# Performance work log

Hardware: AMD Instinct MI355X
Metric: run time of the kernel (lower is better)

The kernel has to match this reference:

```python
import jax, jax.numpy as jnp
import numpy as np
from jax import lax

HID = 256
CB_N = 512   # codebook_size
CB_D = 64    # codebook_dim
FC = 6       # force_channels
COMMIT_W = 0.25


def _conv(x, w, b, stride):
    # x: [B,C,H,W], w: [O,I,3,3], 'same'-style padding=1
    y = lax.conv_general_dilated(x, w, (stride, stride), ((1, 1), (1, 1)),
                                 dimension_numbers=('NCHW', 'OIHW', 'NCHW'))
    return y + b[None, :, None, None]


def _silu(x):
    return x * jax.nn.sigmoid(x)


def setup_inputs() -> dict:
    key = jax.random.key(0)
    ks = jax.random.split(key, 8)
    s = 0.05
    force_field = jax.random.normal(ks[0], (8, FC, 256, 256), dtype=jnp.float32)
    w1 = jax.random.normal(ks[1], (HID, FC, 3, 3), dtype=jnp.float32) * s
    b1 = jnp.zeros((HID,), dtype=jnp.float32)
    w2 = jax.random.normal(ks[2], (HID, HID, 3, 3), dtype=jnp.float32) * s
    b2 = jnp.zeros((HID,), dtype=jnp.float32)
    w3 = jax.random.normal(ks[3], (CB_D, HID, 3, 3), dtype=jnp.float32) * s
    b3 = jnp.zeros((CB_D,), dtype=jnp.float32)
    codebook = jax.random.uniform(ks[4], (CB_N, CB_D), dtype=jnp.float32,
                                  minval=-1.0 / CB_N, maxval=1.0 / CB_N)
    return {"force_field": force_field, "w1": w1, "b1": b1, "w2": w2,
            "b2": b2, "w3": w3, "b3": b3, "codebook": codebook}


def reference(force_field, w1, b1, w2, b2, w3, b3, codebook):
    # Encoder: conv(pad1) -> SiLU -> conv(stride2) -> SiLU -> conv(stride2)
    h = _silu(_conv(force_field, w1, b1, 1))
    h = _silu(_conv(h, w2, b2, 2))
    z = _conv(h, w3, b3, 2)                      # [B, CB_D, h, w]
    B, C, hh, ww = z.shape
    z_flat = jnp.transpose(z, (0, 2, 3, 1)).reshape(-1, C)  # [N, CB_D]
    # pairwise squared distances: ||z||^2 + ||c||^2 - 2 z.c
    dists = (jnp.sum(z_flat * z_flat, axis=1, keepdims=True)
             + jnp.sum(codebook * codebook, axis=1)
             - 2.0 * (z_flat @ codebook.T))      # [N, CB_N]
    indices = jnp.argmin(dists, axis=1)          # [N] int
    z_q = codebook[indices].reshape(B, hh, ww, C).transpose(0, 3, 1, 2)
    commitment_loss = (jnp.mean((lax.stop_gradient(z_q) - z) ** 2)
                       + COMMIT_W * jnp.mean((z_q - lax.stop_gradient(z)) ** 2))
    tokens = indices.reshape(B, hh, ww)
    return tokens, commitment_loss
```

## Files before the change

kernel.cpp:

```cpp
#include <hip/hip_runtime.h>
#include <math.h>


#define FC    6
#define HID   256
#define CB_N  512
#define CB_D  64

typedef _Float16 f16x8 __attribute__((ext_vector_type(8)));
typedef _Float16 f16x4 __attribute__((ext_vector_type(4)));
typedef float f32x16 __attribute__((ext_vector_type(16)));

#define H1N_IMG    17105920
#define H2N_IMG    4359168

#define FFP_ROW    260
#define FFP_CI     (258 * FFP_ROW)
#define FFP_IMG    (6 * FFP_CI)

__global__ void fill_sentinel_kernel(float* out, int n) {
    int i = blockIdx.x * 256 + threadIdx.x;
    if (i < n) out[i] = -12345.0f;
}

__global__ void guards_kernel(unsigned int* h1n, unsigned int* h2n, int nslots) {
    int i = blockIdx.x * 256 + threadIdx.x;
    const int n1 = nslots * 132096;
    if (i < n1) {
        int slot = i / 132096;
        int r    = i - slot * 132096;
        unsigned int* base = h1n + (size_t)slot * H1N_IMG;
        if (r < 66560) base[r] = 0u;
        else {
            int r2  = r - 66560;
            int j   = r2 & 3;
            int hl  = (r2 >> 2) & 1;
            int cg  = (r2 >> 3) & 31;
            int row = (r2 >> 8) + 1;
            base[(size_t)row * 66560 + 33280 + cg * 1040 + hl * 520 + j] = 0u;
        }
        return;
    }
    i -= n1;
    if (i >= nslots * 66560) return;
    int slot = i / 66560;
    int r    = i - slot * 66560;
    unsigned int* base = h2n + (size_t)slot * H2N_IMG;
    if (r < 33792) base[r] = 0u;
    else {
        int r2  = r - 33792;
        int j   = r2 & 3;
        int hl  = (r2 >> 2) & 1;
        int cg  = (r2 >> 3) & 31;
        int row = (r2 >> 8) + 1;
        base[(size_t)row * 33792 + 16896 + cg * 528 + hl * 264 + j] = 0u;
    }
}

__global__ void wswz1_kernel(const float* __restrict__ w1, _Float16* __restrict__ wsz) {
    int i = blockIdx.x * 256 + threadIdx.x;
    if (i >= 2 * 4 * 4096) return;
    int j   = i & 7;
    int co_ = (i >> 3) & 127;
    int kc  = (i >> 10) & 1;
    int hf  = (i >> 11) & 1;
    int st  = (i >> 12) & 3;
    int ct  = i >> 14;
    int k   = st * 16 + kc * 8 + j;
    int co  = ct * 128 + co_;
    float v = (k < 54) ? w1[(size_t)co * 54 + k] : 0.f;
    _Float16 h = (_Float16)v;
    _Float16 l = (_Float16)(v - (float)h);
    wsz[i] = hf ? l : h;
}

__global__ void wswz2_kernel(const float* __restrict__ w2, _Float16* __restrict__ wsz) {
    int i = blockIdx.x * 256 + threadIdx.x;
    if (i >= 2 * 144 * 4096) return;
    int j   = i & 7;
    int co_ = (i >> 3) & 127;
    int kc  = (i >> 10) & 1;
    int hf  = (i >> 11) & 1;
    int st  = (i >> 12) % 144;
    int ct  = (i >> 12) / 144;
    int ci  = (st & 15) * 16 + kc * 8 + j;
    int rs  = st >> 4;
    float v = w2[(size_t)(ct * 128 + co_) * 2304 + ci * 9 + rs];
    _Float16 h = (_Float16)v;
    _Float16 l = (_Float16)(v - (float)h);
    wsz[i] = hf ? l : h;
}

__global__ void wswz3_kernel(const float* __restrict__ w3, _Float16* __restrict__ wsz) {
    int i = blockIdx.x * 256 + threadIdx.x;
    if (i >= 144 * 2048) return;
    int j  = i & 7;
    int co = (i >> 3) & 63;
    int kc = (i >> 9) & 1;
    int hf = (i >> 10) & 1;
    int st = i >> 11;
    int ci = (st & 15) * 16 + kc * 8 + j;
    int rs = st >> 4;
    float v = w3[(size_t)co * 2304 + ci * 9 + rs];
    _Float16 h = (_Float16)v;
    _Float16 l = (_Float16)(v - (float)h);
    wsz[i] = hf ? l : h;
}

__global__ void cnorm_kernel(const float* __restrict__ cb, float* __restrict__ cn) {
    int j = blockIdx.x * 256 + threadIdx.x;
    if (j < CB_N) {
        const float* p = cb + j * CB_D;
        float s0 = 0.f, s1 = 0.f, s2 = 0.f, s3 = 0.f;
        for (int i = 0; i < CB_D; i += 4) {
            s0 = fmaf(p[i],   p[i],   s0);
            s1 = fmaf(p[i+1], p[i+1], s1);
            s2 = fmaf(p[i+2], p[i+2], s2);
            s3 = fmaf(p[i+3], p[i+3], s3);
        }
        cn[j] = (s0 + s1) + (s2 + s3);
    }
}

__device__ __forceinline__ float silu_f(float v) {
    return v / (1.f + expf(-v));
}

__device__ __forceinline__ unsigned int pack_hl(float v) {
    _Float16 h = (_Float16)v;
    _Float16 l = (_Float16)(v - (float)h);
    unsigned short hb = __builtin_bit_cast(unsigned short, h);
    unsigned short lb = __builtin_bit_cast(unsigned short, l);
    return (unsigned int)hb | ((unsigned int)lb << 16);
}

__device__ __forceinline__ f16x8 as_f16x8(uint4 v) {
    return __builtin_bit_cast(f16x8, v);
}

__device__ __forceinline__ unsigned int ldu32_sb(const char* base, unsigned off, int px) {
    return *(const unsigned int*)(base + (unsigned)__builtin_amdgcn_readfirstlane((int)off) + px * 4);
}

__device__ __forceinline__ void sync_lds() {
    asm volatile("s_waitcnt lgkmcnt(0)\n\ts_barrier" ::: "memory");
}

__global__ __launch_bounds__(256) void ffpack_kernel(const float* __restrict__ ff,
                                                     unsigned int* __restrict__ ffp) {
    const int gw   = (blockIdx.x * 256 + threadIdx.x) >> 6;
    const int lane = threadIdx.x & 63;
    const int y  = gw & 255;
    const int ic = gw >> 8;
    const float* rowp = ff + ((size_t)ic * 256 + y) * 256;
    float4 v = *(const float4*)(rowp + 4 * lane);
    unsigned p0 = pack_hl(v.x), p1 = pack_hl(v.y), p2 = pack_hl(v.z), p3 = pack_hl(v.w);
    unsigned p3p = __shfl_up(p3, 1);
    if (lane == 0) p3p = 0u;
    unsigned int* orow = ffp + ((size_t)ic * 258 + y + 1) * FFP_ROW;
    uint4 o; o.x = p3p; o.y = p0; o.z = p1; o.w = p2;
    *(uint4*)(orow + 4 * lane) = o;
    if (lane == 63) { orow[256] = p3; orow[257] = 0u; }
}

__global__ __launch_bounds__(256) void conv1_mfma_kernel(
        const unsigned int* __restrict__ ffp,
        const _Float16* __restrict__ wsz1,
        const float* __restrict__ bias,
        unsigned int* __restrict__ h1n,
        int b0) {
    __shared__ __align__(16) _Float16 ldsA[2][2][128][8];
    __shared__ __align__(16) _Float16 ldsB[2][128][24];
    __shared__ __align__(16) unsigned int T[64];
    __shared__ float biasl[128];

    const int tid = threadIdx.x;
    const int py  = blockIdx.x >> 1;
    const int xt  = blockIdx.x & 1;
    const int ct  = blockIdx.y;
    const int img = blockIdx.z;

    const unsigned int* ffpi = ffp + (size_t)(b0 + img) * FFP_IMG;
    _Float16* h1f = (_Float16*)(h1n + (size_t)img * H1N_IMG);

    if (tid < 64) {
        int k = tid;
        unsigned off;
        if (k < 54) {
            int ci  = k / 9;
            int tap = k - ci * 9;
            int r   = tap / 3;
            int s   = tap - r * 3;
            off = (unsigned)((((size_t)ci * 258 + py + r) * FFP_ROW + xt * 128 + s) * 4);
        } else {
            off = (unsigned)((xt * 128) * 4);
        }
        T[k] = off;
    }
    if (tid < 128) biasl[tid] = bias[ct * 128 + tid];
    __syncthreads();

    const int lane = tid & 63;
    const int w    = tid >> 6;
    const int cow  = (w >> 1) * 64;
    const int pxw  = (w & 1) * 64;
    const int m_   = lane & 31;
    const int kc   = lane >> 5;
    const int px   = tid & 127;
    const int kh   = tid >> 7;

    f32x16 acc[2][2];
    #pragma unroll
    for (int a = 0; a < 2; a++)
        #pragma unroll
        for (int b = 0; b < 2; b++)
            #pragma unroll
            for (int r = 0; r < 16; r++) acc[a][b][r] = 0.f;

    uint4* aldsf = (uint4*)&ldsA[0][0][0][0];
    const char* gbase = (const char*)ffpi;

    uint4 a0, a1;
    unsigned v0, v1, v2, v3, v4, v5, v6, v7;
    {
        const uint4* ag = (const uint4*)(wsz1 + ((size_t)(ct * 4)) * 4096);
        a0 = ag[tid];
        a1 = ag[tid + 256];
        const int k0 = kh * 8;
        uint4 rb0 = *(const uint4*)&T[k0];
        uint4 rb1 = *(const uint4*)&T[k0 + 4];
        v0 = ldu32_sb(gbase, rb0.x, px); v1 = ldu32_sb(gbase, rb0.y, px);
        v2 = ldu32_sb(gbase, rb0.z, px); v3 = ldu32_sb(gbase, rb0.w, px);
        v4 = ldu32_sb(gbase, rb1.x, px); v5 = ldu32_sb(gbase, rb1.y, px);
        v6 = ldu32_sb(gbase, rb1.z, px); v7 = ldu32_sb(gbase, rb1.w, px);
    }

    for (int t = 0; t < 4; t++) {
        sync_lds();

        aldsf[tid]       = a0;
        aldsf[tid + 256] = a1;
        uint4 bh, bl;
        bh.x = (v0 & 0xffffu) | (v1 << 16);
        bh.y = (v2 & 0xffffu) | (v3 << 16);
        bh.z = (v4 & 0xffffu) | (v5 << 16);
        bh.w = (v6 & 0xffffu) | (v7 << 16);
        bl.x = (v0 >> 16) | (v1 & 0xffff0000u);
        bl.y = (v2 >> 16) | (v3 & 0xffff0000u);
        bl.z = (v4 >> 16) | (v5 & 0xffff0000u);
        bl.w = (v6 >> 16) | (v7 & 0xffff0000u);
        *(uint4*)&ldsB[0][px][kh * 8] = bh;
        *(uint4*)&ldsB[1][px][kh * 8] = bl;

        sync_lds();

        if (t < 3) {
            const uint4* ag = (const uint4*)(wsz1 + ((size_t)(ct * 4 + t + 1)) * 4096);
            a0 = ag[tid];
            a1 = ag[tid + 256];
            const int k0 = (t + 1) * 16 + kh * 8;
            uint4 rb0 = *(const uint4*)&T[k0 & 63];
            uint4 rb1 = *(const uint4*)&T[(k0 + 4) & 63];
            v0 = ldu32_sb(gbase, rb0.x, px); v1 = ldu32_sb(gbase, rb0.y, px);
            v2 = ldu32_sb(gbase, rb0.z, px); v3 = ldu32_sb(gbase, rb0.w, px);
            v4 = ldu32_sb(gbase, rb1.x, px); v5 = ldu32_sb(gbase, rb1.y, px);
            v6 = ldu32_sb(gbase, rb1.z, px); v7 = ldu32_sb(gbase, rb1.w, px);
        }

        f16x8 ah0 = *(const f16x8*)&ldsA[0][kc][cow + m_][0];
        f16x8 ah1 = *(const f16x8*)&ldsA[0][kc][cow + 32 + m_][0];
        f16x8 al0 = *(const f16x8*)&ldsA[1][kc][cow + m_][0];
        f16x8 al1 = *(const f16x8*)&ldsA[1][kc][cow + 32 + m_][0];
        f16x8 xh0 = *(const f16x8*)&ldsB[0][pxw + m_][kc * 8];
        f16x8 xh1 = *(const f16x8*)&ldsB[0][pxw + 32 + m_][kc * 8];
        f16x8 xl0 = *(const f16x8*)&ldsB[1][pxw + m_][kc * 8];
        f16x8 xl1 = *(const f16x8*)&ldsB[1][pxw + 32 + m_][kc * 8];

        acc[0][0] = __builtin_amdgcn_mfma_f32_32x32x16_f16(ah0, xh0, acc[0][0], 0, 0, 0);
        acc[0][1] = __builtin_amdgcn_mfma_f32_32x32x16_f16(ah0, xh1, acc[0][1], 0, 0, 0);
        acc[1][0] = __builtin_amdgcn_mfma_f32_32x32x16_f16(ah1, xh0, acc[1][0], 0, 0, 0);
        acc[1][1] = __builtin_amdgcn_mfma_f32_32x32x16_f16(ah1, xh1, acc[1][1], 0, 0, 0);
        acc[0][0] = __builtin_amdgcn_mfma_f32_32x32x16_f16(ah0, xl0, acc[0][0], 0, 0, 0);
        acc[0][1] = __builtin_amdgcn_mfma_f32_32x32x16_f16(ah0, xl1, acc[0][1], 0, 0, 0);
        acc[1][0] = __builtin_amdgcn_mfma_f32_32x32x16_f16(ah1, xl0, acc[1][0], 0, 0, 0);
        acc[1][1] = __builtin_amdgcn_mfma_f32_32x32x16_f16(ah1, xl1, acc[1][1], 0, 0, 0);
        acc[0][0] = __builtin_amdgcn_mfma_f32_32x32x16_f16(al0, xh0, acc[0][0], 0, 0, 0);
        acc[0][1] = __builtin_amdgcn_mfma_f32_32x32x16_f16(al0, xh1, acc[0][1], 0, 0, 0);
        acc[1][0] = __builtin_amdgcn_mfma_f32_32x32x16_f16(al1, xh0, acc[1][0], 0, 0, 0);
        acc[1][1] = __builtin_amdgcn_mfma_f32_32x32x16_f16(al1, xh1, acc[1][1], 0, 0, 0);
    }

    #pragma unroll
    for (int mt = 0; mt < 2; mt++) {
        #pragma unroll
        for (int nt = 0; nt < 2; nt++) {
            const int pxo = xt * 128 + pxw + nt * 32 + m_;
            const int par = pxo & 1;
            const int xs  = par ? ((pxo + 1) >> 1) : (pxo >> 1);
            _Float16* dst = h1f + (size_t)(py + 1) * 133120 + par * 66560 + xs * 8 + kc * 4;
            #pragma unroll
            for (int q = 0; q < 4; q++) {
                const int cb_ = cow + mt * 32 + 8 * q + 4 * kc;
                const int cg  = (ct * 128 + cow + mt * 32 + 8 * q) >> 3;
                f16x4 oh, ol;
                #pragma unroll
                for (int j = 0; j < 4; j++) {
                    float v = silu_f(acc[mt][nt][4*q+j] + biasl[cb_ + j]);
                    _Float16 h = (_Float16)v;
                    oh[j] = h;
                    ol[j] = (_Float16)(v - (float)h);
                }
                *(f16x4*)(dst + (size_t)cg * 2080)        = oh;
                *(f16x4*)(dst + (size_t)cg * 2080 + 1040) = ol;
            }
        }
    }
}

__global__ __launch_bounds__(256) void conv2_mfma_kernel(
        const unsigned int* __restrict__ h1n,
        const _Float16* __restrict__ wsz2,
        const float* __restrict__ bias,
        unsigned int* __restrict__ h2n) {
    __shared__ __align__(16) char ldsB[2 * 16384];
    __shared__ float biasl[128];

    const int tid = threadIdx.x;
    const int py  = blockIdx.x;
    const int ct  = blockIdx.y;
    const int img = blockIdx.z;

    if (tid < 128) biasl[tid] = bias[ct * 128 + tid];

    const int lane = tid & 63;
    const int w    = tid >> 6;
    const int cow  = (w >> 1) * 64;
    const int pxw  = (w & 1) * 64;
    const int m_   = lane & 31;
    const int kc   = lane >> 5;

    const char* bbase = (const char*)(h1n + (size_t)img * H1N_IMG);
    const char* abase = (const char*)wsz2 + (size_t)ct * 144 * 8192
                        + (size_t)kc * 2048 + (size_t)(cow + m_) * 16;

    const int spx = tid & 127;
    const int skc = tid >> 7;
    const unsigned sgfix = (unsigned)(skc * 4160 + spx * 16);
    const unsigned swfix = (unsigned)(skc * 2048 + spx * 16);
    const unsigned rfix0 = (unsigned)(kc * 2048 + (pxw + m_) * 16);
    const unsigned rfix1 = (unsigned)(kc * 2048 + (pxw + 32 + m_) * 16);

    auto offu = [&](int t) -> unsigned {
        int rs = t >> 4;
        int r  = (rs * 11) >> 5;
        int s  = rs - 3 * r;
        return (unsigned)((2 * py + r) * 266240 + (s != 1 ? 133120 : 0)
                          + (s == 2 ? 16 : 0) + (t & 15) * 8320);
    };

    f32x16 acc[2][2];
    #pragma unroll
    for (int a = 0; a < 2; a++)
        #pragma unroll
        for (int b = 0; b < 2; b++)
            #pragma unroll
            for (int r = 0; r < 16; r++) acc[a][b][r] = 0.f;

    uint4 pa0, pa1, pa2, pa3;
    uint4 wa0, wa1, wa2, wa3;
    uint4 wb0, wb1, wb2, wb3;
    {
        pa0 = *(const uint4*)(abase);
        pa1 = *(const uint4*)(abase + 512);
        pa2 = *(const uint4*)(abase + 4096);
        pa3 = *(const uint4*)(abase + 4096 + 512);
        unsigned o0 = offu(0);
        uint4 th = *(const uint4*)(bbase + o0 + sgfix);
        uint4 tl = *(const uint4*)(bbase + o0 + sgfix + 2080);
        *(uint4*)(ldsB + swfix)        = th;
        *(uint4*)(ldsB + 4096 + swfix) = tl;
        unsigned o1 = offu(1);
        th = *(const uint4*)(bbase + o1 + sgfix);
        tl = *(const uint4*)(bbase + o1 + sgfix + 2080);
        *(uint4*)(ldsB + 8192 + swfix)  = th;
        *(uint4*)(ldsB + 12288 + swfix) = tl;
        unsigned o2 = offu(2);
        wa0 = *(const uint4*)(bbase + o2 + sgfix);
        wa1 = *(const uint4*)(bbase + o2 + sgfix + 2080);
        unsigned o3 = offu(3);
        wa2 = *(const uint4*)(bbase + o3 + sgfix);
        wa3 = *(const uint4*)(bbase + o3 + sgfix + 2080);
        unsigned o4 = offu(4);
        wb0 = *(const uint4*)(bbase + o4 + sgfix);
        wb1 = *(const uint4*)(bbase + o4 + sgfix + 2080);
        unsigned o5 = offu(5);
        wb2 = *(const uint4*)(bbase + o5 + sgfix);
        wb3 = *(const uint4*)(bbase + o5 + sgfix + 2080);
    }
    sync_lds();

    auto superstep = [&](int s, uint4& W0, uint4& W1, uint4& W2, uint4& W3) {
        const int t0 = 2 * s;
        char* rslot = ldsB + (s & 1) * 16384;

        if (s < 71) {
            char* wslot = ldsB + ((s + 1) & 1) * 16384;
            *(uint4*)(wslot + swfix)         = W0;
            *(uint4*)(wslot + 4096 + swfix)  = W1;
            *(uint4*)(wslot + 8192 + swfix)  = W2;
            *(uint4*)(wslot + 12288 + swfix) = W3;
        }
        if (s < 69) {
            unsigned oa = offu(t0 + 6);
            unsigned ob = offu(t0 + 7);
            W0 = *(const uint4*)(bbase + oa + sgfix);
            W1 = *(const uint4*)(bbase + oa + sgfix + 2080);
            W2 = *(const uint4*)(bbase + ob + sgfix);
            W3 = *(const uint4*)(bbase + ob + sgfix + 2080);
        }

        f16x8 xh0 = *(const f16x8*)(rslot + rfix0);
        f16x8 xl0 = *(const f16x8*)(rslot + 4096 + rfix0);
        f16x8 xh1 = *(const f16x8*)(rslot + rfix1);
        f16x8 xl1 = *(const f16x8*)(rslot + 4096 + rfix1);

        uint4 ca0 = pa0, ca1 = pa1, ca2 = pa2, ca3 = pa3;
        {
            const char* ap = abase + (size_t)(t0 + 1) * 8192;
            pa0 = *(const uint4*)(ap);
            pa1 = *(const uint4*)(ap + 512);
            pa2 = *(const uint4*)(ap + 4096);
            pa3 = *(const uint4*)(ap + 4096 + 512);
        }

        f16x8 ah0 = as_f16x8(ca0);
        f16x8 ah1 = as_f16x8(ca1);
        f16x8 al0 = as_f16x8(ca2);
        f16x8 al1 = as_f16x8(ca3);

        acc[0][0] = __builtin_amdgcn_mfma_f32_32x32x16_f16(ah0, xh0, acc[0][0], 0, 0, 0);
        acc[0][1] = __builtin_amdgcn_mfma_f32_32x32x16_f16(ah0, xh1, acc[0][1], 0, 0, 0);
        acc[1][0] = __builtin_amdgcn_mfma_f32_32x32x16_f16(ah1, xh0, acc[1][0], 0, 0, 0);
        acc[1][1] = __builtin_amdgcn_mfma_f32_32x32x16_f16(ah1, xh1, acc[1][1], 0, 0, 0);
        acc[0][0] = __builtin_amdgcn_mfma_f32_32x32x16_f16(ah0, xl0, acc[0][0], 0, 0, 0);
        acc[0][1] = __builtin_amdgcn_mfma_f32_32x32x16_f16(ah0, xl1, acc[0][1], 0, 0, 0);
        acc[1][0] = __builtin_amdgcn_mfma_f32_32x32x16_f16(ah1, xl0, acc[1][0], 0, 0, 0);
        acc[1][1] = __builtin_amdgcn_mfma_f32_32x32x16_f16(ah1, xl1, acc[1][1], 0, 0, 0);
        acc[0][0] = __builtin_amdgcn_mfma_f32_32x32x16_f16(al0, xh0, acc[0][0], 0, 0, 0);
        acc[0][1] = __builtin_amdgcn_mfma_f32_32x32x16_f16(al0, xh1, acc[0][1], 0, 0, 0);
        acc[1][0] = __builtin_amdgcn_mfma_f32_32x32x16_f16(al1, xh0, acc[1][0], 0, 0, 0);
        acc[1][1] = __builtin_amdgcn_mfma_f32_32x32x16_f16(al1, xh1, acc[1][1], 0, 0, 0);

        f16x8 yh0 = *(const f16x8*)(rslot + 8192 + rfix0);
        f16x8 yl0 = *(const f16x8*)(rslot + 12288 + rfix0);
        f16x8 yh1 = *(const f16x8*)(rslot + 8192 + rfix1);
        f16x8 yl1 = *(const f16x8*)(rslot + 12288 + rfix1);

        ca0 = pa0; ca1 = pa1; ca2 = pa2; ca3 = pa3;
        if (s < 71) {
            const char* ap = abase + (size_t)(t0 + 2) * 8192;
            pa0 = *(const uint4*)(ap);
            pa1 = *(const uint4*)(ap + 512);
            pa2 = *(const uint4*)(ap + 4096);
            pa3 = *(const uint4*)(ap + 4096 + 512);
        }

        ah0 = as_f16x8(ca0);
        ah1 = as_f16x8(ca1);
        al0 = as_f16x8(ca2);
        al1 = as_f16x8(ca3);

        acc[0][0] = __builtin_amdgcn_mfma_f32_32x32x16_f16(ah0, yh0, acc[0][0], 0, 0, 0);
        acc[0][1] = __builtin_amdgcn_mfma_f32_32x32x16_f16(ah0, yh1, acc[0][1], 0, 0, 0);
        acc[1][0] = __builtin_amdgcn_mfma_f32_32x32x16_f16(ah1, yh0, acc[1][0], 0, 0, 0);
        acc[1][1] = __builtin_amdgcn_mfma_f32_32x32x16_f16(ah1, yh1, acc[1][1], 0, 0, 0);
        acc[0][0] = __builtin_amdgcn_mfma_f32_32x32x16_f16(ah0, yl0, acc[0][0], 0, 0, 0);
        acc[0][1] = __builtin_amdgcn_mfma_f32_32x32x16_f16(ah0, yl1, acc[0][1], 0, 0, 0);
        acc[1][0] = __builtin_amdgcn_mfma_f32_32x32x16_f16(ah1, yl0, acc[1][0], 0, 0, 0);
        acc[1][1] = __builtin_amdgcn_mfma_f32_32x32x16_f16(ah1, yl1, acc[1][1], 0, 0, 0);
        acc[0][0] = __builtin_amdgcn_mfma_f32_32x32x16_f16(al0, yh0, acc[0][0], 0, 0, 0);
        acc[0][1] = __builtin_amdgcn_mfma_f32_32x32x16_f16(al0, yh1, acc[0][1], 0, 0, 0);
        acc[1][0] = __builtin_amdgcn_mfma_f32_32x32x16_f16(al1, yh0, acc[1][0], 0, 0, 0);
        acc[1][1] = __builtin_amdgcn_mfma_f32_32x32x16_f16(al1, yh1, acc[1][1], 0, 0, 0);

        sync_lds();
    };

    for (int ss = 0; ss < 36; ss++) {
        superstep(2 * ss,     wa0, wa1, wa2, wa3);
        superstep(2 * ss + 1, wb0, wb1, wb2, wb3);
    }

    _Float16* h2f = (_Float16*)(h2n + (size_t)img * H2N_IMG);
    #pragma unroll
    for (int mt = 0; mt < 2; mt++) {
        #pragma unroll
        for (int nt = 0; nt < 2; nt++) {
            const int pxo = pxw + nt * 32 + m_;
            const int par = pxo & 1;
            const int xs  = par ? ((pxo + 1) >> 1) : (pxo >> 1);
            _Float16* dst = h2f + (size_t)(py + 1) * 67584 + par * 33792 + xs * 8 + kc * 4;
            #pragma unroll
            for (int q = 0; q < 4; q++) {
                const int cb_ = cow + mt * 32 + 8 * q + 4 * kc;
                const int cg  = (ct * 128 + cow + mt * 32 + 8 * q) >> 3;
                f16x4 oh, ol;
                #pragma unroll
                for (int j = 0; j < 4; j++) {
                    float v = silu_f(acc[mt][nt][4*q+j] + biasl[cb_ + j]);
                    _Float16 h = (_Float16)v;
                    oh[j] = h;
                    ol[j] = (_Float16)(v - (float)h);
                }
                *(f16x4*)(dst + (size_t)cg * 1056)       = oh;
                *(f16x4*)(dst + (size_t)cg * 1056 + 528) = ol;
            }
        }
    }
}

__global__ __launch_bounds__(64) void conv3_mfma_kernel(
        const unsigned int* __restrict__ h2n,
        const _Float16* __restrict__ wsz3,
        const float* __restrict__ bias,
        float* __restrict__ z) {
    const int bi  = blockIdx.x;
    const int img = blockIdx.y;
    const int py  = bi >> 2;
    const int ct3 = (bi >> 1) & 1;
    const int pxt = bi & 1;

    const int lane = threadIdx.x;
    const int m_   = lane & 31;
    const int kc   = lane >> 5;

    const char* bbase = (const char*)(h2n + (size_t)img * H2N_IMG);
    const char* abase = (const char*)wsz3 + (size_t)kc * 1024 + (size_t)(ct3 * 32 + m_) * 16;
    const unsigned bfix = (unsigned)(kc * 2112 + (pxt * 32 + m_) * 16);

    auto offu = [&](int t) -> unsigned {
        int rs = t >> 4;
        int r  = (rs * 11) >> 5;
        int s  = rs - 3 * r;
        return (unsigned)((2 * py + r) * 135168 + (s != 1 ? 67584 : 0)
                          + (s == 2 ? 16 : 0) + (t & 15) * 4224);
    };

    f32x16 acc;
    #pragma unroll
    for (int r = 0; r < 16; r++) acc[r] = 0.f;

    uint4 rh[8], rl[8];
    #pragma unroll
    for (int i = 0; i < 8; i++) {
        unsigned o = offu(i);
        rh[i] = *(const uint4*)(bbase + o + bfix);
        rl[i] = *(const uint4*)(bbase + o + bfix + 1056);
    }
    uint4 pa0 = *(const uint4*)(abase);
    uint4 pa1 = *(const uint4*)(abase + 2048);

    for (int tb = 0; tb < 144; tb += 8) {
        #pragma unroll
        for (int i = 0; i < 8; i++) {
            const int t = tb + i;
            uint4 cbh = rh[i], cbl = rl[i];
            if (t + 8 < 144) {
                unsigned o = offu(t + 8);
                rh[i] = *(const uint4*)(bbase + o + bfix);
                rl[i] = *(const uint4*)(bbase + o + bfix + 1056);
            }
            uint4 ca0 = pa0, ca1 = pa1;
            if (t < 143) {
                const char* ap = abase + (size_t)(t + 1) * 4096;
                pa0 = *(const uint4*)(ap);
                pa1 = *(const uint4*)(ap + 2048);
            }
            f16x8 ah = as_f16x8(ca0);
            f16x8 al = as_f16x8(ca1);
            f16x8 xh = as_f16x8(cbh);
            f16x8 xl = as_f16x8(cbl);
            acc = __builtin_amdgcn_mfma_f32_32x32x16_f16(ah, xh, acc, 0, 0, 0);
            acc = __builtin_amdgcn_mfma_f32_32x32x16_f16(ah, xl, acc, 0, 0, 0);
            acc = __builtin_amdgcn_mfma_f32_32x32x16_f16(al, xh, acc, 0, 0, 0);
        }
    }

    const int x = pxt * 32 + m_;
    float* zp = z + (((size_t)img * 64 + py) * 64 + x) * 64;
    #pragma unroll
    for (int q = 0; q < 4; q++) {
        const int co = ct3 * 32 + 8 * q + 4 * kc;
        float4 o;
        o.x = acc[4*q+0] + bias[co + 0];
        o.y = acc[4*q+1] + bias[co + 1];
        o.z = acc[4*q+2] + bias[co + 2];
        o.w = acc[4*q+3] + bias[co + 3];
        *(float4*)(zp + co) = o;
    }
}

__global__ __launch_bounds__(128) void vqfused_kernel(const float* __restrict__ z,
                                                      const float* __restrict__ cb,
                                                      const float* __restrict__ cn,
                                                      float* __restrict__ tokens_out,
                                                      float* __restrict__ loss_accum) {
    __shared__ __align__(16) float lds_cb[128 * 64];
    __shared__ float lds_cn[128];
    __shared__ float red[2];

    const int tid = threadIdx.x;
    const int n   = blockIdx.x * 128 + tid;

    float zr[64];
    const float* zp = z + (size_t)n * 64;
    #pragma unroll
    for (int i = 0; i < 16; i++)
        *(float4*)&zr[i * 4] = *(const float4*)(zp + i * 4);

    float zn0 = 0.f, zn1 = 0.f, zn2 = 0.f, zn3 = 0.f;
    #pragma unroll
    for (int i = 0; i < 64; i += 4) {
        zn0 = fmaf(zr[i],   zr[i],   zn0);
        zn1 = fmaf(zr[i+1], zr[i+1], zn1);
        zn2 = fmaf(zr[i+2], zr[i+2], zn2);
        zn3 = fmaf(zr[i+3], zr[i+3], zn3);
    }
    const float znorm = (zn0 + zn1) + (zn2 + zn3);

    float dmin = 1e30f;
    int best = 0;

    for (int q = 0; q < 4; q++) {
        if (q) __syncthreads();
        #pragma unroll
        for (int i = 0; i < 16; i++) {
            const int f4 = tid + 128 * i;
            *(float4*)&lds_cb[f4 * 4] = *(const float4*)(cb + q * 8192 + f4 * 4);
        }
        lds_cn[tid] = cn[q * 128 + tid];
        __syncthreads();

        for (int j = 0; j < 128; j++) {
            const float* cp = &lds_cb[j * 64];
            float d0 = 0.f, d1 = 0.f, d2 = 0.f, d3 = 0.f;
            #pragma unroll
            for (int i = 0; i < 16; i++) {
                const float4 c4 = *(const float4*)&cp[i * 4];
                d0 = fmaf(zr[i*4],   c4.x, d0);
                d1 = fmaf(zr[i*4+1], c4.y, d1);
                d2 = fmaf(zr[i*4+2], c4.z, d2);
                d3 = fmaf(zr[i*4+3], c4.w, d3);
            }
            const float dot = (d0 + d1) + (d2 + d3);
            const float d = (znorm + lds_cn[j]) - 2.f * dot;
            if (d < dmin) { dmin = d; best = q * 128 + j; }
        }
    }

    tokens_out[n] = (float)best;

    const float* cbest = cb + (size_t)best * 64;
    float l0 = 0.f, l1 = 0.f, l2 = 0.f, l3 = 0.f;
    #pragma unroll
    for (int i = 0; i < 64; i += 4) {
        float t0 = cbest[i]     - zr[i];
        float t1 = cbest[i + 1] - zr[i + 1];
        float t2 = cbest[i + 2] - zr[i + 2];
        float t3 = cbest[i + 3] - zr[i + 3];
        l0 = fmaf(t0, t0, l0);
        l1 = fmaf(t1, t1, l1);
        l2 = fmaf(t2, t2, l2);
        l3 = fmaf(t3, t3, l3);
    }
    float l = (l0 + l1) + (l2 + l3);
    #pragma unroll
    for (int off = 32; off > 0; off >>= 1)
        l += __shfl_down(l, off);
    if ((tid & 63) == 0) red[tid >> 6] = l;
    __syncthreads();
    if (tid == 0)
        atomicAdd(loss_accum, red[0] + red[1]);
}

__global__ void finalize_kernel(const float* __restrict__ loss_accum,
                                float* __restrict__ out_loss) {
    const float m = loss_accum[0] / 2097152.f;
    out_loss[0] = m + 0.25f * m;
}

extern "C" void kernel_launch(void* const* d_in, const int* in_sizes, int n_in,
                              void* d_out, int out_size, void* d_ws, size_t ws_size,
                              hipStream_t stream) {
    const float* ff = (const float*)d_in[0];
    const float* w1 = (const float*)d_in[1];
    const float* b1 = (const float*)d_in[2];
    const float* w2 = (const float*)d_in[3];
    const float* b2 = (const float*)d_in[4];
    const float* w3 = (const float*)d_in[5];
    const float* b3 = (const float*)d_in[6];
    const float* cb = (const float*)d_in[7];
    float* out = (float*)d_out;
    float* ws  = (float*)d_ws;

    const size_t TAIL = 2097152 + 8 * (size_t)FFP_IMG + 589824 + 147456 + 16384
                      + 512 + 131072 + 131072 + 1;
    auto need_u32 = [&](int nimg) -> size_t {
        return (size_t)nimg * (H1N_IMG + H2N_IMG) + TAIL;
    };

    int nimg;
    if      (ws_size >= need_u32(8) * 4) nimg = 8;
    else if (ws_size >= need_u32(4) * 4) nimg = 4;
    else if (ws_size >= need_u32(2) * 4) nimg = 2;
    else {
        fill_sentinel_kernel<<<(out_size + 255) / 256, 256, 0, stream>>>(out, out_size);
        return;
    }

    unsigned int* h1n  = (unsigned int*)ws;
    unsigned int* h2n  = h1n + (size_t)nimg * H1N_IMG;
    float*        zbuf = (float*)(h2n + (size_t)nimg * H2N_IMG);
    unsigned int* ffp  = (unsigned int*)(zbuf + 2097152);
    _Float16* wsz2 = (_Float16*)(ffp + 8 * (size_t)FFP_IMG);
    _Float16* wsz3 = wsz2 + 1179648;
    _Float16* wsz1 = wsz3 + 294912;
    float*    cn   = (float*)(wsz1 + 32768);
    float*    pd   = cn + 512;
    int*      pi   = (int*)(pd + 131072);
    float*    lacc = (float*)(pi + 131072);

    hipMemsetAsync(ffp, 0, 8 * (size_t)FFP_IMG * 4, stream);
    guards_kernel<<<(nimg * (132096 + 66560) + 255) / 256, 256, 0, stream>>>(h1n, h2n, nimg);
    wswz1_kernel<<<(2 * 4 * 4096 + 255) / 256, 256, 0, stream>>>(w1, wsz1);
    wswz2_kernel<<<(2 * 144 * 4096 + 255) / 256, 256, 0, stream>>>(w2, wsz2);
    wswz3_kernel<<<(144 * 2048 + 255) / 256, 256, 0, stream>>>(w3, wsz3);
    cnorm_kernel<<<2, 256, 0, stream>>>(cb, cn);
    ffpack_kernel<<<3072, 256, 0, stream>>>(ff, ffp);

    for (int b0 = 0; b0 < 8; b0 += nimg) {
        conv1_mfma_kernel<<<dim3(512, 2, nimg), 256, 0, stream>>>(ffp, wsz1, b1, h1n, b0);
        conv2_mfma_kernel<<<dim3(128, 2, nimg), 256, 0, stream>>>(h1n, wsz2, b2, h2n);
        conv3_mfma_kernel<<<dim3(256, nimg), 64, 0, stream>>>(
            h2n, wsz3, b3, zbuf + (size_t)b0 * 262144);
    }

    hipMemsetAsync(lacc, 0, sizeof(float), stream);
    vqfused_kernel<<<256, 128, 0, stream>>>(zbuf, cb, cn, out, lacc);
    finalize_kernel<<<1, 1, 0, stream>>>(lacc, out + 32768);
}
```

Baseline: 953.4 us.

## Split VQ codebook search across two half-blocks and merge prep kernels

The VQ kernel now runs 256 threads per block. Each half searches a different 256-entry half of the codebook for the same 128 vectors, then the two halves merge their minima through shared memory. This doubles the active waves in the latency-bound argmin stage, at the cost of each thread loading its z row twice and an extra sync. The four weight-swizzle and codebook-norm kernels are also fused into one launch, and the image batch size can now be any value from 2 to 8 depending on workspace.

```diff
diff --git a/kernel.cpp b/kernel.cpp
--- a/kernel.cpp
+++ b/kernel.cpp
@@ -57,68 +57,68 @@
     }
 }
 
-__global__ void wswz1_kernel(const float* __restrict__ w1, _Float16* __restrict__ wsz) {
+__global__ void prep_kernel(const float* __restrict__ w1, const float* __restrict__ w2,
+                            const float* __restrict__ w3, const float* __restrict__ cbk,
+                            _Float16* __restrict__ wsz1, _Float16* __restrict__ wsz2,
+                            _Float16* __restrict__ wsz3, float* __restrict__ cn) {
     int i = blockIdx.x * 256 + threadIdx.x;
-    if (i >= 2 * 4 * 4096) return;
-    int j   = i & 7;
-    int co_ = (i >> 3) & 127;
-    int kc  = (i >> 10) & 1;
-    int hf  = (i >> 11) & 1;
-    int st  = (i >> 12) & 3;
-    int ct  = i >> 14;
-    int k   = st * 16 + kc * 8 + j;
-    int co  = ct * 128 + co_;
-    float v = (k < 54) ? w1[(size_t)co * 54 + k] : 0.f;
-    _Float16 h = (_Float16)v;
-    _Float16 l = (_Float16)(v - (float)h);
-    wsz[i] = hf ? l : h;
-}
-
-__global__ void wswz2_kernel(const float* __restrict__ w2, _Float16* __restrict__ wsz) {
-    int i = blockIdx.x * 256 + threadIdx.x;
-    if (i >= 2 * 144 * 4096) return;
-    int j   = i & 7;
-    int co_ = (i >> 3) & 127;
-    int kc  = (i >> 10) & 1;
-    int hf  = (i >> 11) & 1;
-    int st  = (i >> 12) % 144;
-    int ct  = (i >> 12) / 144;
-    int ci  = (st & 15) * 16 + kc * 8 + j;
-    int rs  = st >> 4;
-    float v = w2[(size_t)(ct * 128 + co_) * 2304 + ci * 9 + rs];
-    _Float16 h = (_Float16)v;
-    _Float16 l = (_Float16)(v - (float)h);
-    wsz[i] = hf ? l : h;
-}
-
-__global__ void wswz3_kernel(const float* __restrict__ w3, _Float16* __restrict__ wsz) {
-    int i = blockIdx.x * 256 + threadIdx.x;
-    if (i >= 144 * 2048) return;
-    int j  = i & 7;
-    int co = (i >> 3) & 63;
-    int kc = (i >> 9) & 1;
-    int hf = (i >> 10) & 1;
-    int st = i >> 11;
-    int ci = (st & 15) * 16 + kc * 8 + j;
-    int rs = st >> 4;
-    float v = w3[(size_t)co * 2304 + ci * 9 + rs];
-    _Float16 h = (_Float16)v;
-    _Float16 l = (_Float16)(v - (float)h);
-    wsz[i] = hf ? l : h;
-}
-
-__global__ void cnorm_kernel(const float* __restrict__ cb, float* __restrict__ cn) {
-    int j = blockIdx.x * 256 + threadIdx.x;
-    if (j < CB_N) {
-        const float* p = cb + j * CB_D;
+    if (i < 32768) {
+        int j   = i & 7;
+        int co_ = (i >> 3) & 127;
+        int kc  = (i >> 10) & 1;
+        int hf  = (i >> 11) & 1;
+        int st  = (i >> 12) & 3;
+        int ct  = i >> 14;
+        int k   = st * 16 + kc * 8 + j;
+        int co  = ct * 128 + co_;
+        float v = (k < 54) ? w1[(size_t)co * 54 + k] : 0.f;
+        _Float16 h = (_Float16)v;
+        _Float16 l = (_Float16)(v - (float)h);
+        wsz1[i] = hf ? l : h;
+        return;
+    }
+    i -= 32768;
+    if (i < 2 * 144 * 4096) {
+        int j   = i & 7;
+        int co_ = (i >> 3) & 127;
+        int kc  = (i >> 10) & 1;
+        int hf  = (i >> 11) & 1;
+        int st  = (i >> 12) % 144;
+        int ct  = (i >> 12) / 144;
+        int ci  = (st & 15) * 16 + kc * 8 + j;
+        int rs  = st >> 4;
+        float v = w2[(size_t)(ct * 128 + co_) * 2304 + ci * 9 + rs];
+        _Float16 h = (_Float16)v;
+        _Float16 l = (_Float16)(v - (float)h);
+        wsz2[i] = hf ? l : h;
+        return;
+    }
+    i -= 2 * 144 * 4096;
+    if (i < 144 * 2048) {
+        int j  = i & 7;
+        int co = (i >> 3) & 63;
+        int kc = (i >> 9) & 1;
+        int hf = (i >> 10) & 1;
+        int st = i >> 11;
+        int ci = (st & 15) * 16 + kc * 8 + j;
+        int rs = st >> 4;
+        float v = w3[(size_t)co * 2304 + ci * 9 + rs];
+        _Float16 h = (_Float16)v;
+        _Float16 l = (_Float16)(v - (float)h);
+        wsz3[i] = hf ? l : h;
+        return;
+    }
+    i -= 144 * 2048;
+    if (i < CB_N) {
+        const float* p = cbk + i * CB_D;
         float s0 = 0.f, s1 = 0.f, s2 = 0.f, s3 = 0.f;
-        for (int i = 0; i < CB_D; i += 4) {
-            s0 = fmaf(p[i],   p[i],   s0);
-            s1 = fmaf(p[i+1], p[i+1], s1);
-            s2 = fmaf(p[i+2], p[i+2], s2);
-            s3 = fmaf(p[i+3], p[i+3], s3);
-        }
-        cn[j] = (s0 + s1) + (s2 + s3);
+        for (int k = 0; k < CB_D; k += 4) {
+            s0 = fmaf(p[k],   p[k],   s0);
+            s1 = fmaf(p[k+1], p[k+1], s1);
+            s2 = fmaf(p[k+2], p[k+2], s2);
+            s3 = fmaf(p[k+3], p[k+3], s3);
+        }
+        cn[i] = (s0 + s1) + (s2 + s3);
     }
 }
 
@@ -600,17 +600,21 @@
     }
 }
 
-__global__ __launch_bounds__(128) void vqfused_kernel(const float* __restrict__ z,
+__global__ __launch_bounds__(256) void vqfused_kernel(const float* __restrict__ z,
                                                       const float* __restrict__ cb,
                                                       const float* __restrict__ cn,
                                                       float* __restrict__ tokens_out,
                                                       float* __restrict__ loss_accum) {
-    __shared__ __align__(16) float lds_cb[128 * 64];
-    __shared__ float lds_cn[128];
-    __shared__ float red[2];
-
-    const int tid = threadIdx.x;
-    const int n   = blockIdx.x * 128 + tid;
+    __shared__ __align__(16) float lds_cb[2][64 * 64];
+    __shared__ float lds_cn[2][64];
+    __shared__ float lds_d[128];
+    __shared__ int   lds_i[128];
+    __shared__ float red[4];
+
+    const int tid  = threadIdx.x;
+    const int half = tid >> 7;
+    const int ltid = tid & 127;
+    const int n    = blockIdx.x * 128 + ltid;
 
     float zr[64];
     const float* zp = z + (size_t)n * 64;
@@ -631,18 +635,19 @@
     float dmin = 1e30f;
     int best = 0;
 
-    for (int q = 0; q < 4; q++) {
-        if (q) __syncthreads();
+    for (int st = 0; st < 4; st++) {
+        const int c0 = half * 256 + st * 64;
+        if (st) __syncthreads();
         #pragma unroll
-        for (int i = 0; i < 16; i++) {
-            const int f4 = tid + 128 * i;
-            *(float4*)&lds_cb[f4 * 4] = *(const float4*)(cb + q * 8192 + f4 * 4);
-        }
-        lds_cn[tid] = cn[q * 128 + tid];
+        for (int i = 0; i < 8; i++) {
+            const int f4 = ltid + 128 * i;
+            *(float4*)&lds_cb[half][f4 * 4] = *(const float4*)(cb + (size_t)c0 * 64 + f4 * 4);
+        }
+        if (ltid < 64) lds_cn[half][ltid] = cn[c0 + ltid];
         __syncthreads();
 
-        for (int j = 0; j < 128; j++) {
-            const float* cp = &lds_cb[j * 64];
+        for (int j = 0; j < 64; j++) {
+            const float* cp = &lds_cb[half][j * 64];
             float d0 = 0.f, d1 = 0.f, d2 = 0.f, d3 = 0.f;
             #pragma unroll
             for (int i = 0; i < 16; i++) {
@@ -653,34 +658,43 @@
                 d3 = fmaf(zr[i*4+3], c4.w, d3);
             }
             const float dot = (d0 + d1) + (d2 + d3);
-            const float d = (znorm + lds_cn[j]) - 2.f * dot;
-            if (d < dmin) { dmin = d; best = q * 128 + j; }
-        }
-    }
-
-    tokens_out[n] = (float)best;
-
-    const float* cbest = cb + (size_t)best * 64;
-    float l0 = 0.f, l1 = 0.f, l2 = 0.f, l3 = 0.f;
-    #pragma unroll
-    for (int i = 0; i < 64; i += 4) {
-        float t0 = cbest[i]     - zr[i];
-        float t1 = cbest[i + 1] - zr[i + 1];
-        float t2 = cbest[i + 2] - zr[i + 2];
-        float t3 = cbest[i + 3] - zr[i + 3];
-        l0 = fmaf(t0, t0, l0);
-        l1 = fmaf(t1, t1, l1);
-        l2 = fmaf(t2, t2, l2);
-        l3 = fmaf(t3, t3, l3);
-    }
-    float l = (l0 + l1) + (l2 + l3);
+            const float d = (znorm + lds_cn[half][j]) - 2.f * dot;
+            if (d < dmin) { dmin = d; best = c0 + j; }
+        }
+    }
+
+    if (half) { lds_d[ltid] = dmin; lds_i[ltid] = best; }
+    __syncthreads();
+
+    float l = 0.f;
+    if (half == 0) {
+        const float d1 = lds_d[ltid];
+        const int   i1 = lds_i[ltid];
+        if (d1 < dmin) { dmin = d1; best = i1; }
+        tokens_out[n] = (float)best;
+
+        const float* cbest = cb + (size_t)best * 64;
+        float l0 = 0.f, l1 = 0.f, l2 = 0.f, l3 = 0.f;
+        #pragma unroll
+        for (int i = 0; i < 64; i += 4) {
+            float t0 = cbest[i]     - zr[i];
+            float t1 = cbest[i + 1] - zr[i + 1];
+            float t2 = cbest[i + 2] - zr[i + 2];
+            float t3 = cbest[i + 3] - zr[i + 3];
+            l0 = fmaf(t0, t0, l0);
+            l1 = fmaf(t1, t1, l1);
+            l2 = fmaf(t2, t2, l2);
+            l3 = fmaf(t3, t3, l3);
+        }
+        l = (l0 + l1) + (l2 + l3);
+    }
     #pragma unroll
     for (int off = 32; off > 0; off >>= 1)
         l += __shfl_down(l, off);
     if ((tid & 63) == 0) red[tid >> 6] = l;
     __syncthreads();
     if (tid == 0)
-        atomicAdd(loss_accum, red[0] + red[1]);
+        atomicAdd(loss_accum, (red[0] + red[1]) + (red[2] + red[3]));
 }
 
 __global__ void finalize_kernel(const float* __restrict__ loss_accum,
@@ -709,11 +723,11 @@
         return (size_t)nimg * (H1N_IMG + H2N_IMG) + TAIL;
     };
 
-    int nimg;
-    if      (ws_size >= need_u32(8) * 4) nimg = 8;
-    else if (ws_size >= need_u32(4) * 4) nimg = 4;
-    else if (ws_size >= need_u32(2) * 4) nimg = 2;
-    else {
+    int nimg = 0;
+    for (int n = 8; n >= 2; n--) {
+        if (ws_size >= need_u32(n) * 4) { nimg = n; break; }
+    }
+    if (nimg == 0) {
         fill_sentinel_kernel<<<(out_size + 255) / 256, 256, 0, stream>>>(out, out_size);
         return;
     }
@@ -729,23 +743,23 @@
     float*    pd   = cn + 512;
     int*      pi   = (int*)(pd + 131072);
     float*    lacc = (float*)(pi + 131072);
+    (void)pd; (void)pi;
 
     hipMemsetAsync(ffp, 0, 8 * (size_t)FFP_IMG * 4, stream);
     guards_kernel<<<(nimg * (132096 + 66560) + 255) / 256, 256, 0, stream>>>(h1n, h2n, nimg);
-    wswz1_kernel<<<(2 * 4 * 4096 + 255) / 256, 256, 0, stream>>>(w1, wsz1);
-    wswz2_kernel<<<(2 * 144 * 4096 + 255) / 256, 256, 0, stream>>>(w2, wsz2);
-    wswz3_kernel<<<(144 * 2048 + 255) / 256, 256, 0, stream>>>(w3, wsz3);
-    cnorm_kernel<<<2, 256, 0, stream>>>(cb, cn);
+    prep_kernel<<<(1507840 + 255) / 256, 256, 0, stream>>>(w1, w2, w3, cb,
+                                                           wsz1, wsz2, wsz3, cn);
     ffpack_kernel<<<3072, 256, 0, stream>>>(ff, ffp);
 
     for (int b0 = 0; b0 < 8; b0 += nimg) {
-        conv1_mfma_kernel<<<dim3(512, 2, nimg), 256, 0, stream>>>(ffp, wsz1, b1, h1n, b0);
-        conv2_mfma_kernel<<<dim3(128, 2, nimg), 256, 0, stream>>>(h1n, wsz2, b2, h2n);
-        conv3_mfma_kernel<<<dim3(256, nimg), 64, 0, stream>>>(
+        const int cur = (8 - b0 < nimg) ? (8 - b0) : nimg;
+        conv1_mfma_kernel<<<dim3(512, 2, cur), 256, 0, stream>>>(ffp, wsz1, b1, h1n, b0);
+        conv2_mfma_kernel<<<dim3(128, 2, cur), 256, 0, stream>>>(h1n, wsz2, b2, h2n);
+        conv3_mfma_kernel<<<dim3(256, cur), 64, 0, stream>>>(
             h2n, wsz3, b3, zbuf + (size_t)b0 * 262144);
     }
 
     hipMemsetAsync(lacc, 0, sizeof(float), stream);
-    vqfused_kernel<<<256, 128, 0, stream>>>(zbuf, cb, cn, out, lacc);
+    vqfused_kernel<<<256, 256, 0, stream>>>(zbuf, cb, cn, out, lacc);
     finalize_kernel<<<1, 1, 0, stream>>>(lacc, out + 32768);
 }
```

Result: faster. 922.2 us (-3.3%).
